# Kernel optimization log

Measured on AMD Instinct MI355X. Metric: run time of the kernel, lower is better.

The kernel has to match this reference:

```python
import jax, jax.numpy as jnp
import numpy as np

TEMPERATURE = 0.07


def setup_inputs() -> dict:
    key = jax.random.key(0)
    k1, k2 = jax.random.split(key)
    B, D = 4096, 256
    x = jax.random.normal(k1, (B, D), dtype=jnp.float32)
    y = jax.random.normal(k2, (B, D), dtype=jnp.float32)
    # L2-normalize so dot products lie in [-1, 1] (realistic contrastive
    # embeddings; keeps exp(dot / 0.07) finite as the original code assumes).
    x = x / jnp.linalg.norm(x, axis=-1, keepdims=True)
    y = y / jnp.linalg.norm(y, axis=-1, keepdims=True)
    return {"x": x, "y": y}


def reference(x, y):
    # Faithful translation of the (quirky) original loop:
    # for each row i, neg_dot starts at zeros and is filled one j at a time;
    # at EVERY inner step k the code computes exp(neg_dot/T) over the full
    # vector (entries j>k are still 0 -> exp=1) and accumulates
    #   loss += -log(exp[i] / sum(exp)).
    # Vectorized:
    #   S[i,j] = x_i . y_j / T
    #   denom[i,k] = sum_{j<=k} exp(S[i,j]) + (B-1-k)    (zeros contribute e^0)
    #   numer log term: S[i,i] if k>=i else 0 -> contributes (B-i)*S[i,i]
    B = x.shape[0]
    S = jnp.einsum("id,jd->ij", x, y) / TEMPERATURE          # [B, B]
    cumE = jnp.cumsum(jnp.exp(S), axis=1)                     # [B, B]
    k = jnp.arange(B, dtype=S.dtype)
    denom = cumE + (B - 1.0 - k)[None, :]                     # [B, B]
    diag = jnp.diagonal(S)                                    # [B]
    n_hits = (B - jnp.arange(B)).astype(S.dtype)              # k >= i count
    loss = jnp.sum(jnp.log(denom)) - jnp.sum(n_hits * diag)
    return loss
```

## Files before the change

### kernel.cpp

```cpp
#include <hip/hip_runtime.h>

typedef __bf16  bf16x8 __attribute__((ext_vector_type(8)));
typedef short   s16x8  __attribute__((ext_vector_type(8)));
typedef float   f32x4  __attribute__((ext_vector_type(4)));
typedef unsigned short u16;
typedef u16     u16x4  __attribute__((ext_vector_type(4)));
typedef unsigned int u32;

#define B_SZ 4096
#define D_SZ 256

static constexpr float SCALE = (float)(1.4426950408889634 / 0.07);
static constexpr float LN2F  = 0.69314718055994531f;

__device__ __forceinline__ u16 f2bf(float f) {
  unsigned u = __float_as_uint(f);
  unsigned r = u + 0x7FFFu + ((u >> 16) & 1u);
  return (u16)(r >> 16);
}
__device__ __forceinline__ float bf2f(u16 h) {
  return __uint_as_float((u32)h << 16);
}

template<bool BF>
__device__ __forceinline__ bf16x8 ld8(const u16* pb, const float* pf) {
  if constexpr (BF) {
    return *(const bf16x8*)pb;
  } else {
    f32x4 a = *(const f32x4*)pf;
    f32x4 b = *(const f32x4*)(pf + 4);
    s16x8 s;
#pragma unroll
    for (int i = 0; i < 4; ++i) { s[i] = (short)f2bf(a[i]); s[i + 4] = (short)f2bf(b[i]); }
    return __builtin_bit_cast(bf16x8, s);
  }
}

__global__ __launch_bounds__(256) void cl_convert(const float* __restrict__ x,
                                                  const float* __restrict__ y,
                                                  u16* __restrict__ xb,
                                                  u16* __restrict__ yb) {
  const int idx = (int)(blockIdx.x * 256 + threadIdx.x) * 4;
  f32x4 vx = *(const f32x4*)(x + idx);
  f32x4 vy = *(const f32x4*)(y + idx);
  u16x4 sx, sy;
#pragma unroll
  for (int i = 0; i < 4; ++i) { sx[i] = f2bf(vx[i]); sy[i] = f2bf(vy[i]); }
  *(u16x4*)(xb + idx) = sx;
  *(u16x4*)(yb + idx) = sy;
}

__global__ __launch_bounds__(256, 2) void cl_gemm(const u16* __restrict__ xb,
                                                  const u16* __restrict__ yb,
                                                  u16* __restrict__ Sl) {
  __shared__ u16 As[2][128 * 64];
  __shared__ u16 Bs[2][128 * 64];
  const int tid  = threadIdx.x;
  const int lane = tid & 63;
  const int wv   = tid >> 6;
  const int l15  = lane & 15;
  const int lg   = lane >> 4;
  const int wm   = wv >> 1;
  const int wn   = wv & 1;
  int bid = (int)blockIdx.x;
  bid = (bid & 7) * 128 + (bid >> 3);
  const int brow = (bid >> 5) << 7;
  const int bcol = (bid & 31) << 7;

  auto stage_panel = [&](u16* panel, const u16* src, int row0, int kt) {
#pragma unroll
    for (int i = 0; i < 4; ++i) {
      const int chunk = i * 4 + wv;
      const int r = chunk * 8 + (lane >> 3);
      const int cs = ((lane & 7) << 4) ^ ((r & 7) << 4);
      const char* g = (const char*)src + ((size_t)(row0 + r) << 9) + (kt << 7) + cs;
      auto lp = (__attribute__((address_space(3))) u32*)
                  ((char*)panel + chunk * 1024 + lane * 16);
      __builtin_amdgcn_global_load_lds((const __attribute__((address_space(1))) u32*)g,
                                       lp, 16, 0, 0);
    }
  };

  f32x4 acc[4][4] = {};

  stage_panel(As[0], xb, brow, 0);
  stage_panel(Bs[0], yb, bcol, 0);
  __syncthreads();

#pragma unroll 1
  for (int kt = 0; kt < 4; ++kt) {
    if (kt < 3) {
      stage_panel(As[(kt + 1) & 1], xb, brow, kt + 1);
      stage_panel(Bs[(kt + 1) & 1], yb, bcol, kt + 1);
    }
    const u16* Ap = As[kt & 1];
    const u16* Bp = Bs[kt & 1];
    bf16x8 Af[4][2], Bf[4][2];
#pragma unroll
    for (int mi = 0; mi < 4; ++mi)
#pragma unroll
      for (int ks = 0; ks < 2; ++ks) {
        const int ra = (wm << 6) + (mi << 4) + l15;
        const int ca = ((ks << 6) + (lg << 4)) ^ ((ra & 7) << 4);
        Af[mi][ks] = *(const bf16x8*)((const char*)Ap + (ra << 7) + ca);
        const int rb = (wn << 6) + (mi << 4) + l15;
        const int cb = ((ks << 6) + (lg << 4)) ^ ((rb & 7) << 4);
        Bf[mi][ks] = *(const bf16x8*)((const char*)Bp + (rb << 7) + cb);
      }
#pragma unroll
    for (int mi = 0; mi < 4; ++mi)
#pragma unroll
      for (int ni = 0; ni < 4; ++ni)
#pragma unroll
        for (int ks = 0; ks < 2; ++ks)
          acc[mi][ni] = __builtin_amdgcn_mfma_f32_16x16x32_bf16(
              Bf[ni][ks], Af[mi][ks], acc[mi][ni], 0, 0, 0);
    __syncthreads();
  }

#pragma unroll
  for (int mi = 0; mi < 4; ++mi)
#pragma unroll
    for (int ni = 0; ni < 4; ++ni) {
      u16x4 o;
#pragma unroll
      for (int v = 0; v < 4; ++v) o[v] = f2bf(acc[mi][ni][v] * SCALE);
      const int rs = brow + (wm << 6) + (mi << 4) + l15;
      const int cs = bcol + (wn << 6) + (ni << 4) + (lg << 2);
      *(u16x4*)(Sl + (size_t)rs * B_SZ + cs) = o;
    }
}

__global__ __launch_bounds__(256) void cl_scan(const u16* __restrict__ Sl,
                                               float* __restrict__ partials) {
  __shared__ float wtot[4];
  __shared__ float red2[4];
  const int row  = (int)blockIdx.x;
  const int tid  = threadIdx.x;
  const int lane = tid & 63;
  const int wv   = tid >> 6;

  const u16* rp = Sl + (size_t)row * B_SZ + tid * 16;
  s16x8 a = *(const s16x8*)rp;
  s16x8 b = *(const s16x8*)(rp + 8);
  float t[16], p[16];
  float run = 0.f;
#pragma unroll
  for (int j = 0; j < 8; ++j) { t[j] = bf2f((u16)a[j]); t[8 + j] = bf2f((u16)b[j]); }
#pragma unroll
  for (int j = 0; j < 16; ++j) { run += __builtin_amdgcn_exp2f(t[j]); p[j] = run; }

  float s = run;
#pragma unroll
  for (int d = 1; d < 64; d <<= 1) {
    float u = __shfl_up(s, (unsigned)d, 64);
    if (lane >= d) s += u;
  }
  if (lane == 63) wtot[wv] = s;
  __syncthreads();
  float off = 0.f;
#pragma unroll
  for (int w = 0; w < 4; ++w) if (w < wv) off += wtot[w];
  const float excl = off + (s - run);

  float lacc = 0.f;
  const int c0 = tid * 16;
#pragma unroll
  for (int j = 0; j < 16; ++j)
    lacc += __builtin_amdgcn_logf(excl + p[j] + (float)(B_SZ - 1 - (c0 + j)));
  if ((row >> 4) == tid) lacc -= (float)(B_SZ - row) * t[row & 15];
  lacc *= LN2F;

#pragma unroll
  for (int d = 1; d < 64; d <<= 1) lacc += __shfl_xor(lacc, d, 64);
  if (lane == 0) red2[wv] = lacc;
  __syncthreads();
  if (tid == 0)
    partials[row] = (red2[0] + red2[1]) + (red2[2] + red2[3]);
}

__global__ __launch_bounds__(256) void cl_final(const float* __restrict__ p,
                                                float* __restrict__ out) {
  __shared__ float red[256];
  const int tid = threadIdx.x;
  float s = 0.f;
#pragma unroll
  for (int k = 0; k < 16; ++k) s += p[tid + 256 * k];
  red[tid] = s;
  __syncthreads();
#pragma unroll
  for (int o = 128; o > 0; o >>= 1) {
    if (tid < o) red[tid] += red[tid + o];
    __syncthreads();
  }
  if (tid == 0) out[0] = red[0];
}

template<bool BF>
__global__ __launch_bounds__(256) void cl_main(const float* __restrict__ x,
                                               const float* __restrict__ y,
                                               const u16* __restrict__ xb,
                                               const u16* __restrict__ yb,
                                               float* __restrict__ partials) {
  __shared__ float st[16][68];
  __shared__ float red[256];
  const int tid  = threadIdx.x;
  const int lane = tid & 63;
  const int wv   = tid >> 6;
  const int l15  = lane & 15;
  const int lg   = lane >> 4;
  const int i0   = blockIdx.x * 16;

  bf16x8 A[8];
  {
    const size_t base = (size_t)(i0 + l15) * D_SZ + (lg << 3);
#pragma unroll
    for (int ks = 0; ks < 8; ++ks)
      A[ks] = ld8<BF>(xb + base + ks * 32, x + base + ks * 32);
  }

  float lacc = 0.f, carry = 0.f;

  auto load_b = [&](bf16x8 (&F)[8], int t) {
    const size_t jb = (size_t)(t * 64 + (wv << 4) + l15) * D_SZ + (lg << 3);
#pragma unroll
    for (int ks = 0; ks < 8; ++ks)
      F[ks] = ld8<BF>(yb + jb + ks * 32, y + jb + ks * 32);
  };

  auto body = [&](bf16x8 (&F)[8], int t) {
    f32x4 acc = {0.f, 0.f, 0.f, 0.f};
#pragma unroll
    for (int ks = 0; ks < 8; ++ks)
      acc = __builtin_amdgcn_mfma_f32_16x16x32_bf16(A[ks], F[ks], acc, 0, 0, 0);
    __syncthreads();
    const int colg = t * 64 + (wv << 4) + l15;
#pragma unroll
    for (int v = 0; v < 4; ++v) {
      float tv = acc[v] * SCALE;
      const int rowl = (lg << 2) + v;
      if (i0 + rowl == colg) lacc -= (float)(B_SZ - colg) * tv;
      st[rowl][(wv << 4) + l15] = tv;
    }
    __syncthreads();
    const int row = (wv << 2) + lg;
    f32x4 tv4 = *(const f32x4*)&st[row][l15 << 2];
    float e0 = __builtin_amdgcn_exp2f(tv4[0]);
    float e1 = __builtin_amdgcn_exp2f(tv4[1]);
    float e2 = __builtin_amdgcn_exp2f(tv4[2]);
    float e3 = __builtin_amdgcn_exp2f(tv4[3]);
    float p1 = e0 + e1, p2 = p1 + e2, p3 = p2 + e3;
    float s = p3;
#pragma unroll
    for (int d = 1; d < 16; d <<= 1) {
      float u = __shfl_up(s, (unsigned)d, 16);
      if (l15 >= d) s += u;
    }
    const float base = carry + (s - p3);
    const float c0 = (float)(B_SZ - 1 - (t * 64 + (l15 << 2)));
    lacc += __builtin_amdgcn_logf(base + e0 + c0)
          + __builtin_amdgcn_logf(base + p1 + (c0 - 1.f))
          + __builtin_amdgcn_logf(base + p2 + (c0 - 2.f))
          + __builtin_amdgcn_logf(base + p3 + (c0 - 3.f));
    carry += __shfl(s, 15, 16);
  };

  bf16x8 B0[8], B1[8];
  load_b(B0, 0);
#pragma unroll 1
  for (int t2 = 0; t2 < 32; ++t2) {
    const int t0 = t2 * 2;
    load_b(B1, t0 + 1);
    body(B0, t0);
    if (t0 + 2 < 64) load_b(B0, t0 + 2);
    body(B1, t0 + 1);
  }

  red[tid] = lacc * LN2F;
  __syncthreads();
#pragma unroll
  for (int o = 128; o > 0; o >>= 1) {
    if (tid < o) red[tid] += red[tid + o];
    __syncthreads();
  }
  if (tid == 0) partials[blockIdx.x] = red[0];
}

__global__ __launch_bounds__(256) void cl_reduce(const float* __restrict__ p,
                                                 float* __restrict__ out) {
  __shared__ float red[256];
  const int tid = threadIdx.x;
  red[tid] = p[tid];
  __syncthreads();
#pragma unroll
  for (int o = 128; o > 0; o >>= 1) {
    if (tid < o) red[tid] += red[tid + o];
    __syncthreads();
  }
  if (tid == 0) out[0] = red[0];
}

extern "C" void kernel_launch(void* const* d_in, const int* in_sizes, int n_in,
                              void* d_out, int out_size, void* d_ws, size_t ws_size,
                              hipStream_t stream) {
  const float* x = (const float*)d_in[0];
  const float* y = (const float*)d_in[1];
  float* out = (float*)d_out;
  const size_t BD = (size_t)B_SZ * D_SZ;

  float* partials = (float*)d_ws;
  u16* xb = (u16*)((char*)d_ws + 16384 + 256);
  u16* yb = xb + BD;
  u16* Sl = yb + BD;
  const size_t need = 16384 + 256 + 4 * BD + 2 * (size_t)B_SZ * B_SZ;

  if (ws_size >= need) {
    cl_convert<<<(int)(BD / 1024), 256, 0, stream>>>(x, y, xb, yb);
    cl_gemm<<<1024, 256, 0, stream>>>(xb, yb, Sl);
    cl_scan<<<B_SZ, 256, 0, stream>>>(Sl, partials);
    cl_final<<<1, 256, 0, stream>>>(partials, out);
  } else {
    float* fpart = (float*)d_ws;
    u16* fxb = (u16*)((char*)d_ws + 4096);
    u16* fyb = fxb + BD;
    const size_t fneed = 4096 + 4 * BD;
    if (ws_size >= fneed) {
      cl_convert<<<(int)(BD / 1024), 256, 0, stream>>>(x, y, fxb, fyb);
      cl_main<true><<<B_SZ / 16, 256, 0, stream>>>(x, y, fxb, fyb, fpart);
    } else {
      cl_main<false><<<B_SZ / 16, 256, 0, stream>>>(x, y, fxb, fyb, fpart);
    }
    cl_reduce<<<1, 256, 0, stream>>>(fpart, out);
  }
}
```

Before: 42.48 us.

## Enlarge GEMM block tile to 256x256 with 8 waves and precomputed LDS offsets

Replaces the 128x128-tile, 4-wave GEMM with a 256x256-tile, 8-wave kernel, each wave computing a 64x128 sub-tile with 32 accumulators. It also precomputes the global and LDS address offsets so the inner loop does less index arithmetic. The larger tile is meant to raise data reuse per byte loaded and cut the global traffic for the Sl GEMM. In exchange it uses 128KB of LDS per block and more accumulator registers, and launches only 256 blocks on a 256-CU part, so occupancy and load balance may suffer.

```diff
diff --git a/kernel.cpp b/kernel.cpp
--- a/kernel.cpp
+++ b/kernel.cpp
@@ -50,83 +50,89 @@
   *(u16x4*)(yb + idx) = sy;
 }
 
-__global__ __launch_bounds__(256, 2) void cl_gemm(const u16* __restrict__ xb,
-                                                  const u16* __restrict__ yb,
-                                                  u16* __restrict__ Sl) {
-  __shared__ u16 As[2][128 * 64];
-  __shared__ u16 Bs[2][128 * 64];
+__global__ __launch_bounds__(512, 2) void cl_gemm2(const u16* __restrict__ xb,
+                                                   const u16* __restrict__ yb,
+                                                   u16* __restrict__ Sl) {
+  __shared__ u16 As[2][256 * 64];
+  __shared__ u16 Bs[2][256 * 64];
   const int tid  = threadIdx.x;
   const int lane = tid & 63;
   const int wv   = tid >> 6;
   const int l15  = lane & 15;
   const int lg   = lane >> 4;
-  const int wm   = wv >> 1;
-  const int wn   = wv & 1;
+  const int wr   = wv >> 1;
+  const int wc   = wv & 1;
   int bid = (int)blockIdx.x;
-  bid = (bid & 7) * 128 + (bid >> 3);
-  const int brow = (bid >> 5) << 7;
-  const int bcol = (bid & 31) << 7;
-
-  auto stage_panel = [&](u16* panel, const u16* src, int row0, int kt) {
+  bid = (bid & 7) * 32 + (bid >> 3);
+  const int brow = (bid >> 4) << 8;
+  const int bcol = (bid & 15) << 8;
+
+  const int rsub = (wv << 3) + (lane >> 3);
+  const u32 cs0  = (u32)(((lane & 7) << 4) ^ ((lane >> 3) << 4));
+  const char* aBase = (const char*)xb + ((size_t)(brow + rsub) << 9) + cs0;
+  const char* bBase = (const char*)yb + ((size_t)(bcol + rsub) << 9) + cs0;
+  const u32 dstOff = (u32)((wv << 10) + lane * 16);
+
+  auto stage = [&](u16* panel, const char* base, int kt) {
 #pragma unroll
     for (int i = 0; i < 4; ++i) {
-      const int chunk = i * 4 + wv;
-      const int r = chunk * 8 + (lane >> 3);
-      const int cs = ((lane & 7) << 4) ^ ((r & 7) << 4);
-      const char* g = (const char*)src + ((size_t)(row0 + r) << 9) + (kt << 7) + cs;
+      const char* g = base + i * 32768 + (kt << 7);
       auto lp = (__attribute__((address_space(3))) u32*)
-                  ((char*)panel + chunk * 1024 + lane * 16);
-      __builtin_amdgcn_global_load_lds((const __attribute__((address_space(1))) u32*)g,
-                                       lp, 16, 0, 0);
+                  ((char*)panel + i * 8192 + dstOff);
+      __builtin_amdgcn_global_load_lds(
+          (const __attribute__((address_space(1))) u32*)g, lp, 16, 0, 0);
     }
   };
 
-  f32x4 acc[4][4] = {};
-
-  stage_panel(As[0], xb, brow, 0);
-  stage_panel(Bs[0], yb, bcol, 0);
+  const u32 rowOffA = (u32)((((wr << 6) + l15) << 7));
+  const u32 rowOffB = (u32)((((wc << 7) + l15) << 7));
+  u32 colk[2];
+#pragma unroll
+  for (int ks = 0; ks < 2; ++ks)
+    colk[ks] = (u32)(((ks << 6) + (lg << 4)) ^ ((l15 & 7) << 4));
+
+  f32x4 acc[4][8] = {};
+
+  stage(As[0], aBase, 0);
+  stage(Bs[0], bBase, 0);
   __syncthreads();
 
 #pragma unroll 1
   for (int kt = 0; kt < 4; ++kt) {
     if (kt < 3) {
-      stage_panel(As[(kt + 1) & 1], xb, brow, kt + 1);
-      stage_panel(Bs[(kt + 1) & 1], yb, bcol, kt + 1);
-    }
-    const u16* Ap = As[kt & 1];
-    const u16* Bp = Bs[kt & 1];
-    bf16x8 Af[4][2], Bf[4][2];
-#pragma unroll
-    for (int mi = 0; mi < 4; ++mi)
-#pragma unroll
-      for (int ks = 0; ks < 2; ++ks) {
-        const int ra = (wm << 6) + (mi << 4) + l15;
-        const int ca = ((ks << 6) + (lg << 4)) ^ ((ra & 7) << 4);
-        Af[mi][ks] = *(const bf16x8*)((const char*)Ap + (ra << 7) + ca);
-        const int rb = (wn << 6) + (mi << 4) + l15;
-        const int cb = ((ks << 6) + (lg << 4)) ^ ((rb & 7) << 4);
-        Bf[mi][ks] = *(const bf16x8*)((const char*)Bp + (rb << 7) + cb);
-      }
-#pragma unroll
-    for (int mi = 0; mi < 4; ++mi)
-#pragma unroll
-      for (int ni = 0; ni < 4; ++ni)
-#pragma unroll
-        for (int ks = 0; ks < 2; ++ks)
+      stage(As[(kt + 1) & 1], aBase, kt + 1);
+      stage(Bs[(kt + 1) & 1], bBase, kt + 1);
+    }
+    const char* Ap = (const char*)As[kt & 1];
+    const char* Bp = (const char*)Bs[kt & 1];
+#pragma unroll
+    for (int ks = 0; ks < 2; ++ks) {
+      bf16x8 Af[4], Bf[8];
+      const char* ap = Ap + rowOffA + colk[ks];
+      const char* bp = Bp + rowOffB + colk[ks];
+#pragma unroll
+      for (int mi = 0; mi < 4; ++mi) Af[mi] = *(const bf16x8*)(ap + mi * 2048);
+#pragma unroll
+      for (int ni = 0; ni < 8; ++ni) Bf[ni] = *(const bf16x8*)(bp + ni * 2048);
+#pragma unroll
+      for (int mi = 0; mi < 4; ++mi)
+#pragma unroll
+        for (int ni = 0; ni < 8; ++ni)
           acc[mi][ni] = __builtin_amdgcn_mfma_f32_16x16x32_bf16(
-              Bf[ni][ks], Af[mi][ks], acc[mi][ni], 0, 0, 0);
+              Bf[ni], Af[mi], acc[mi][ni], 0, 0, 0);
+    }
     __syncthreads();
   }
 
 #pragma unroll
   for (int mi = 0; mi < 4; ++mi)
 #pragma unroll
-    for (int ni = 0; ni < 4; ++ni) {
+    for (int ni = 0; ni < 8; ++ni) {
       u16x4 o;
 #pragma unroll
       for (int v = 0; v < 4; ++v) o[v] = f2bf(acc[mi][ni][v] * SCALE);
-      const int rs = brow + (wm << 6) + (mi << 4) + l15;
-      const int cs = bcol + (wn << 6) + (ni << 4) + (lg << 2);
+      const int rs = brow + (wr << 6) + (mi << 4) + l15;
+      const int cs = bcol + (wc << 7) + (ni << 4) + (lg << 2);
       *(u16x4*)(Sl + (size_t)rs * B_SZ + cs) = o;
     }
 }
@@ -316,7 +322,7 @@
 
   if (ws_size >= need) {
     cl_convert<<<(int)(BD / 1024), 256, 0, stream>>>(x, y, xb, yb);
-    cl_gemm<<<1024, 256, 0, stream>>>(xb, yb, Sl);
+    cl_gemm2<<<256, 512, 0, stream>>>(xb, yb, Sl);
     cl_scan<<<B_SZ, 256, 0, stream>>>(Sl, partials);
     cl_final<<<1, 256, 0, stream>>>(partials, out);
   } else {
```

New measurement: 40.57 us. 1.05x faster.

## Single-buffer GEMM LDS to raise occupancy to four blocks per CU

Applied to the files above, without the earlier changes.

The GEMM drops its double-buffered LDS panels in favour of a single buffer, which halves shared memory so launch bounds can request four blocks per CU. It also hoists the swizzled LDS address math and loads fragments per k-slice to cut register pressure. Overlap of global loads with MFMA inside a block is lost and must come from other resident blocks instead. The scan kernel's diagonal subtraction is rewritten as an unrolled per-element check, which avoids dynamic indexing into the register array.

```diff
diff --git a/kernel.cpp b/kernel.cpp
--- a/kernel.cpp
+++ b/kernel.cpp
@@ -50,11 +50,11 @@
   *(u16x4*)(yb + idx) = sy;
 }
 
-__global__ __launch_bounds__(256, 2) void cl_gemm(const u16* __restrict__ xb,
-                                                  const u16* __restrict__ yb,
-                                                  u16* __restrict__ Sl) {
-  __shared__ u16 As[2][128 * 64];
-  __shared__ u16 Bs[2][128 * 64];
+__global__ __launch_bounds__(256, 4) void cl_gemm4(const u16* __restrict__ xb,
+                                                   const u16* __restrict__ yb,
+                                                   u16* __restrict__ Sl) {
+  __shared__ u16 As[128 * 64];
+  __shared__ u16 Bs[128 * 64];
   const int tid  = threadIdx.x;
   const int lane = tid & 63;
   const int wv   = tid >> 6;
@@ -67,55 +67,55 @@
   const int brow = (bid >> 5) << 7;
   const int bcol = (bid & 31) << 7;
 
-  auto stage_panel = [&](u16* panel, const u16* src, int row0, int kt) {
+  const int r0  = (lane >> 3);
+  const u32 cs0 = (u32)(((lane & 7) << 4) ^ (r0 << 4));
+  const u32 dstOff = (u32)(lane * 16);
+
+  auto stage = [&](u16* panel, const u16* src, int row0, int kt) {
 #pragma unroll
     for (int i = 0; i < 4; ++i) {
       const int chunk = i * 4 + wv;
-      const int r = chunk * 8 + (lane >> 3);
-      const int cs = ((lane & 7) << 4) ^ ((r & 7) << 4);
-      const char* g = (const char*)src + ((size_t)(row0 + r) << 9) + (kt << 7) + cs;
+      const int r = chunk * 8 + r0;
+      const char* g = (const char*)src + ((size_t)(row0 + r) << 9)
+                      + (kt << 7) + cs0;
       auto lp = (__attribute__((address_space(3))) u32*)
-                  ((char*)panel + chunk * 1024 + lane * 16);
-      __builtin_amdgcn_global_load_lds((const __attribute__((address_space(1))) u32*)g,
-                                       lp, 16, 0, 0);
+                  ((char*)panel + chunk * 1024 + dstOff);
+      __builtin_amdgcn_global_load_lds(
+          (const __attribute__((address_space(1))) u32*)g, lp, 16, 0, 0);
     }
   };
 
+  const u32 rowOffA = (u32)((((wm << 6) + l15) << 7));
+  const u32 rowOffB = (u32)((((wn << 6) + l15) << 7));
+  u32 colk[2];
+#pragma unroll
+  for (int ks = 0; ks < 2; ++ks)
+    colk[ks] = (u32)(((ks << 6) + (lg << 4)) ^ ((l15 & 7) << 4));
+
   f32x4 acc[4][4] = {};
-
-  stage_panel(As[0], xb, brow, 0);
-  stage_panel(Bs[0], yb, bcol, 0);
-  __syncthreads();
 
 #pragma unroll 1
   for (int kt = 0; kt < 4; ++kt) {
-    if (kt < 3) {
-      stage_panel(As[(kt + 1) & 1], xb, brow, kt + 1);
-      stage_panel(Bs[(kt + 1) & 1], yb, bcol, kt + 1);
-    }
-    const u16* Ap = As[kt & 1];
-    const u16* Bp = Bs[kt & 1];
-    bf16x8 Af[4][2], Bf[4][2];
-#pragma unroll
-    for (int mi = 0; mi < 4; ++mi)
-#pragma unroll
-      for (int ks = 0; ks < 2; ++ks) {
-        const int ra = (wm << 6) + (mi << 4) + l15;
-        const int ca = ((ks << 6) + (lg << 4)) ^ ((ra & 7) << 4);
-        Af[mi][ks] = *(const bf16x8*)((const char*)Ap + (ra << 7) + ca);
-        const int rb = (wn << 6) + (mi << 4) + l15;
-        const int cb = ((ks << 6) + (lg << 4)) ^ ((rb & 7) << 4);
-        Bf[mi][ks] = *(const bf16x8*)((const char*)Bp + (rb << 7) + cb);
-      }
-#pragma unroll
-    for (int mi = 0; mi < 4; ++mi)
-#pragma unroll
-      for (int ni = 0; ni < 4; ++ni)
-#pragma unroll
-        for (int ks = 0; ks < 2; ++ks)
+    if (kt > 0) __syncthreads();
+    stage(As, xb, brow, kt);
+    stage(Bs, yb, bcol, kt);
+    __syncthreads();
+#pragma unroll
+    for (int ks = 0; ks < 2; ++ks) {
+      bf16x8 Af[4], Bf[4];
+      const char* ap = (const char*)As + rowOffA + colk[ks];
+      const char* bp = (const char*)Bs + rowOffB + colk[ks];
+#pragma unroll
+      for (int mi = 0; mi < 4; ++mi) Af[mi] = *(const bf16x8*)(ap + mi * 2048);
+#pragma unroll
+      for (int ni = 0; ni < 4; ++ni) Bf[ni] = *(const bf16x8*)(bp + ni * 2048);
+#pragma unroll
+      for (int mi = 0; mi < 4; ++mi)
+#pragma unroll
+        for (int ni = 0; ni < 4; ++ni)
           acc[mi][ni] = __builtin_amdgcn_mfma_f32_16x16x32_bf16(
-              Bf[ni][ks], Af[mi][ks], acc[mi][ni], 0, 0, 0);
-    __syncthreads();
+              Bf[ni], Af[mi], acc[mi][ni], 0, 0, 0);
+    }
   }
 
 #pragma unroll
@@ -168,7 +168,9 @@
 #pragma unroll
   for (int j = 0; j < 16; ++j)
     lacc += __builtin_amdgcn_logf(excl + p[j] + (float)(B_SZ - 1 - (c0 + j)));
-  if ((row >> 4) == tid) lacc -= (float)(B_SZ - row) * t[row & 15];
+#pragma unroll
+  for (int j = 0; j < 16; ++j)
+    if (row == c0 + j) lacc -= (float)(B_SZ - row) * t[j];
   lacc *= LN2F;
 
 #pragma unroll
@@ -316,7 +318,7 @@
 
   if (ws_size >= need) {
     cl_convert<<<(int)(BD / 1024), 256, 0, stream>>>(x, y, xb, yb);
-    cl_gemm<<<1024, 256, 0, stream>>>(xb, yb, Sl);
+    cl_gemm4<<<1024, 256, 0, stream>>>(xb, yb, Sl);
     cl_scan<<<B_SZ, 256, 0, stream>>>(Sl, partials);
     cl_final<<<1, 256, 0, stream>>>(partials, out);
   } else {
```

Measured after the change: 41.18 us. 1.03x faster.
